# Optimization experiments

Measured on AMD Instinct MI355X. Metric: run time of the kernel, lower is better.

## Reference

```python
import jax, jax.numpy as jnp
import numpy as np

T, B, I, H = 1024, 64, 512, 512


def setup_inputs() -> dict:
    key = jax.random.key(0)
    ks = jax.random.split(key, 7)
    s = 1.0 / np.sqrt(H).astype(np.float32)
    return {
        "x": jax.random.normal(ks[0], (T, B, I), dtype=jnp.float32),
        "h0": jax.random.normal(ks[1], (B, H), dtype=jnp.float32),
        "c0": jax.random.normal(ks[2], (B, H), dtype=jnp.float32),
        "W_ih": jax.random.normal(ks[3], (4 * H, I), dtype=jnp.float32) * s,
        "W_hh": jax.random.normal(ks[4], (4 * H, H), dtype=jnp.float32) * s,
        "b_ih": jax.random.normal(ks[5], (4 * H,), dtype=jnp.float32) * s,
        "b_hh": jax.random.normal(ks[6], (4 * H,), dtype=jnp.float32) * s,
        "alpha": jnp.ones((1,), dtype=jnp.float32),
    }


def reference(x, h0, c0, W_ih, W_hh, b_ih, b_hh, alpha):
    # Precompute input-to-hidden projections for all timesteps in one GEMM.
    # x: [T, B, I] -> xg: [T, B, 4H]
    xg = jnp.einsum("tbi,gi->tbg", x, W_ih) + b_ih
    a = alpha[0]

    def step(carry, xg_t):
        h, c = carry  # [B, H] each
        gates = xg_t + h @ W_hh.T + b_hh  # [B, 4H]
        i, f, g, o = jnp.split(gates, 4, axis=-1)
        i = jax.nn.sigmoid(i)
        f = jax.nn.sigmoid(f)
        g = jnp.tanh(g)
        o = jax.nn.sigmoid(o)
        c_new = f * c + i * g
        h_new = o * jnp.tanh(c_new)
        # alpha step-size interpolation (alpha=1 -> plain LSTM)
        c_out = a * c_new + (1.0 - a) * c
        h_out = a * h_new + (1.0 - a) * h
        return (h_out, c_out), h_out

    (hT, cT), ys = jax.lax.scan(step, (h0, c0), xg)
    return ys, hT, cT
```

## Files before the change

### kernel.cpp

```cpp
#include <hip/hip_runtime.h>

typedef __attribute__((ext_vector_type(8))) short short8;
typedef __attribute__((ext_vector_type(4))) float f32x4;
typedef __attribute__((ext_vector_type(4))) float float4v;
typedef __attribute__((ext_vector_type(4))) unsigned short u16x4;
typedef __attribute__((ext_vector_type(4))) unsigned int u32x4;

#define T_TOT   1024
#define BATCH   64
#define HID     512
#define G4      2048
#define NGRID   128
#define BH      (BATCH * HID)

static __device__ __forceinline__ unsigned short f2bf(float x) {
  union { float f; unsigned u; } v; v.f = x;
  unsigned r = v.u + 0x7FFFu + ((v.u >> 16) & 1u);
  return (unsigned short)(r >> 16);
}
static __device__ __forceinline__ float sigm(float x) {
  return 1.0f / (1.0f + __expf(-x));
}
static __device__ __forceinline__ float tanh_fast(float x) {
  return 1.0f - 2.0f / (__expf(2.0f * x) + 1.0f);
}
static __device__ __forceinline__ void bar_lds() {
  asm volatile("s_waitcnt lgkmcnt(0)" ::: "memory");
  __builtin_amdgcn_s_barrier();
  asm volatile("" ::: "memory");
}

__global__ void init_k(const float* __restrict__ h0, const float* __restrict__ c0,
                       unsigned int* __restrict__ hb2, float* __restrict__ cst,
                       float* __restrict__ hst) {
  const int i = blockIdx.x * 256 + threadIdx.x;
  if (i < BH) {
    const float h = h0[i];
    hb2[i] = (unsigned)f2bf(h);
    hb2[BH + i] = 0xFFFF0000u;
    hst[i] = h;
    cst[i] = c0[i];
  }
}

static __device__ __forceinline__ void gemm_body(
    int bm, int bn, const float* __restrict__ A, const float* __restrict__ W,
    const float* __restrict__ bih, const float* __restrict__ bhh,
    float* __restrict__ xzp) {
  __shared__ unsigned short As[128 * 64];
  __shared__ unsigned short Bs[128 * 64];
  const int tid  = threadIdx.x;
  const int lane = tid & 63;
  const int wid  = tid >> 6;
  const int wm   = (wid >> 1) * 64;
  const int wn   = (wid & 1) * 64;
  const int l15  = lane & 15;
  const int l4   = lane >> 4;

  f32x4 acc[4][4];
#pragma unroll
  for (int mt = 0; mt < 4; ++mt)
#pragma unroll
    for (int nt = 0; nt < 4; ++nt) acc[mt][nt] = f32x4{0.f, 0.f, 0.f, 0.f};

  const float* Ab = A + (long)bm * 128 * 512;
  const float* Wb = W + (long)bn * 128 * 512;
  const int r0 = tid >> 4;
  const int cq = (tid & 15) * 4;

  for (int k0 = 0; k0 < 512; k0 += 64) {
#pragma unroll
    for (int pass = 0; pass < 8; ++pass) {
      const int r = pass * 16 + r0;
      const float4v va = *(const float4v*)(Ab + (long)r * 512 + k0 + cq);
      const float4v vb = *(const float4v*)(Wb + (long)r * 512 + k0 + cq);
      u16x4 pa, pb;
#pragma unroll
      for (int j = 0; j < 4; ++j) { pa[j] = f2bf(va[j]); pb[j] = f2bf(vb[j]); }
      const int boff = r * 128 + ((cq * 2) ^ ((r & 7) << 4));
      *(u16x4*)((char*)As + boff) = pa;
      *(u16x4*)((char*)Bs + boff) = pb;
    }
    __syncthreads();
#pragma unroll
    for (int kk = 0; kk < 2; ++kk) {
      short8 af[4], bfv[4];
#pragma unroll
      for (int mt = 0; mt < 4; ++mt) {
        const int row = wm + mt * 16 + l15;
        af[mt] = *(const short8*)((const char*)As + row * 128 +
                                  ((kk * 64 + l4 * 16) ^ ((row & 7) << 4)));
      }
#pragma unroll
      for (int nt = 0; nt < 4; ++nt) {
        const int row = wn + nt * 16 + l15;
        bfv[nt] = *(const short8*)((const char*)Bs + row * 128 +
                                   ((kk * 64 + l4 * 16) ^ ((row & 7) << 4)));
      }
#pragma unroll
      for (int mt = 0; mt < 4; ++mt)
#pragma unroll
        for (int nt = 0; nt < 4; ++nt)
          acc[mt][nt] = __builtin_amdgcn_mfma_f32_16x16x32_bf16(af[mt], bfv[nt], acc[mt][nt], 0, 0, 0);
    }
    __syncthreads();
  }

#pragma unroll
  for (int nt = 0; nt < 4; ++nt) {
    const int gn = bn * 128 + wn + nt * 16 + l15;
    const float bias = bih[gn] + bhh[gn];
    const int g2  = gn >> 9;
    const int hh  = gn & 511;
    const int nb2 = hh >> 4;
    const int en2 = hh & 15;
#pragma unroll
    for (int mt = 0; mt < 4; ++mt) {
      const int m0 = bm * 128 + wm + mt * 16 + l4 * 4;
#pragma unroll
      for (int r = 0; r < 4; ++r) {
        const int m = m0 + r;
        const int tt2 = m >> 6, brow = m & 63;
        const int mb2 = brow >> 4, em2 = brow & 15;
        xzp[((((size_t)tt2 * 4 + mb2) * 32 + nb2) << 10) + em2 * 64 + g2 * 16 + en2] =
            acc[mt][nt][r] + bias;
      }
    }
  }
}

__global__ __launch_bounds__(256) void xz_gemm(
    const float* __restrict__ A, const float* __restrict__ W,
    const float* __restrict__ bih, const float* __restrict__ bhh,
    float* __restrict__ xzp) {
  gemm_body(blockIdx.x, blockIdx.y, A, W, bih, bhh, xzp);
}

__global__ __launch_bounds__(256, 1) void fused_chunk(
    const float* __restrict__ xnext,
    const float* __restrict__ Wih,
    const float* __restrict__ bih, const float* __restrict__ bhh,
    float* __restrict__ xzp_next,
    const float* __restrict__ xzp_cur,
    const float* __restrict__ Whh,
    const float* __restrict__ alpha_p,
    float* __restrict__ out,
    unsigned int* __restrict__ hb2,
    float* __restrict__ cst, float* __restrict__ hst,
    int t0, int Tc) {
  const int bx = blockIdx.x;
  if (bx >= NGRID) {
    const int g = bx - NGRID;
    gemm_body(g >> 4, g & 15, xnext, Wih, bih, bhh, xzp_next);
    return;
  }

  const int mb  = bx >> 5;
  const int nb  = bx & 31;
  const int rb0 = mb * 16;
  const int hs0 = nb * 16;
  const int tid = threadIdx.x;
  const int lane = tid & 63;
  const int w   = tid >> 6;
  const int l15 = lane & 15;
  const int l4  = lane >> 4;

  __shared__ __align__(16) unsigned short h_lds[16 * HID];
  __shared__ __align__(16) float gates[4][16][20];

  short8 wf[16];
  {
    const float* wr = Whh + (long)(w * HID + hs0 + l15) * HID + l4 * 8;
#pragma unroll
    for (int ks = 0; ks < 16; ++ks) {
      const float4v lo = *(const float4v*)(wr + ks * 32);
      const float4v hi = *(const float4v*)(wr + ks * 32 + 4);
      short8 f;
#pragma unroll
      for (int j = 0; j < 4; ++j) {
        f[j]     = (short)f2bf(lo[j]);
        f[j + 4] = (short)f2bf(hi[j]);
      }
      wf[ks] = f;
    }
  }
  const float a = alpha_p[0];
  const float oma = 1.0f - a;

  const int em = tid >> 4;
  const int en = tid & 15;
  float cp = cst[(long)(rb0 + em) * HID + hs0 + en];
  float hp = hst[(long)(rb0 + em) * HID + hs0 + en];

  const long YS = (long)T_TOT * BATCH * HID;

  float xz0, xz1, xz2, xz3;
  u32x4 sa[4], sb[4];
  {
    const float* xb = xzp_cur + (((size_t)0 * 4 + mb) * 32 + nb) * 1024 + w * 16 + l15;
    asm volatile("global_load_dword %0, %1, off" : "=v"(xz0) : "v"(xb + (l4 * 4 + 0) * 64));
    asm volatile("global_load_dword %0, %1, off" : "=v"(xz1) : "v"(xb + (l4 * 4 + 1) * 64));
    asm volatile("global_load_dword %0, %1, off" : "=v"(xz2) : "v"(xb + (l4 * 4 + 2) * 64));
    asm volatile("global_load_dword %0, %1, off" : "=v"(xz3) : "v"(xb + (l4 * 4 + 3) * 64));
    const unsigned int* p0 = hb2 + (size_t)(t0 & 1) * BH + (size_t)(rb0 + w) * HID + lane * 8;
#pragma unroll
    for (int i = 0; i < 4; ++i) {
      const unsigned int* p = p0 + (size_t)i * 4 * HID;
      asm volatile("global_load_dwordx4 %0, %1, off sc0 sc1" : "=v"(sa[i]) : "v"(p));
      asm volatile("global_load_dwordx4 %0, %1, off sc0 sc1" : "=v"(sb[i]) : "v"(p + 4));
    }
  }

  for (int tt = 0; tt < Tc; ++tt) {
    const int t = t0 + tt;

    if (tt == 0) asm volatile("s_waitcnt vmcnt(0)" ::: "memory");
    else         asm volatile("s_waitcnt vmcnt(1)" ::: "memory");
    __builtin_amdgcn_sched_barrier(0);

    {
      const unsigned wantHi = ((unsigned)t) << 16;
      const unsigned int* p0 = hb2 + (size_t)(t & 1) * BH +
                               (size_t)(rb0 + w) * HID + lane * 8;
      for (;;) {
        unsigned bad = 0u;
#pragma unroll
        for (int i = 0; i < 4; ++i) {
          unsigned d = 0u;
#pragma unroll
          for (int j = 0; j < 4; ++j)
            d |= ((sa[i][j] ^ wantHi) | (sb[i][j] ^ wantHi));
          if (d & 0xFFFF0000u) bad |= (1u << i);
        }
        if (!__any(bad != 0u)) break;
#pragma unroll
        for (int i = 0; i < 4; ++i)
          if (bad & (1u << i)) {
            const unsigned int* p = p0 + (size_t)i * 4 * HID;
            asm volatile("global_load_dwordx4 %0, %1, off sc0 sc1" : "=v"(sa[i]) : "v"(p));
            asm volatile("global_load_dwordx4 %0, %1, off sc0 sc1" : "=v"(sb[i]) : "v"(p + 4));
          }
        asm volatile("s_waitcnt vmcnt(0)" ::: "memory");
        __builtin_amdgcn_sched_barrier(0);
      }
    }

#pragma unroll
    for (int i = 0; i < 4; ++i) {
      u32x4 pk;
      pk[0] = __builtin_amdgcn_perm(sa[i][1], sa[i][0], 0x05040100u);
      pk[1] = __builtin_amdgcn_perm(sa[i][3], sa[i][2], 0x05040100u);
      pk[2] = __builtin_amdgcn_perm(sb[i][1], sb[i][0], 0x05040100u);
      pk[3] = __builtin_amdgcn_perm(sb[i][3], sb[i][2], 0x05040100u);
      const int r = 4 * i + w;
      const int c = lane;
      *(u32x4*)((char*)h_lds + c * 256 + ((r ^ (c & 15)) << 4)) = pk;
    }
    bar_lds();

    f32x4 acc[4];
    acc[0][0] = xz0; acc[0][1] = xz1; acc[0][2] = xz2; acc[0][3] = xz3;
    acc[1] = f32x4{0.f, 0.f, 0.f, 0.f};
    acc[2] = acc[1];
    acc[3] = acc[1];
#pragma unroll
    for (int ks = 0; ks < 16; ++ks) {
      const int c = ks * 4 + l4;
      const short8 af = *(const short8*)((const char*)h_lds + c * 256 +
                                         ((l15 ^ (c & 15)) << 4));
      acc[ks & 3] = __builtin_amdgcn_mfma_f32_16x16x32_bf16(af, wf[ks], acc[ks & 3], 0, 0, 0);
    }
    {
      const f32x4 s = (acc[0] + acc[1]) + (acc[2] + acc[3]);
#pragma unroll
      for (int r = 0; r < 4; ++r)
        gates[w][l4 * 4 + r][l15] = s[r];
    }
    bar_lds();

    const float gi = gates[0][em][en], gf = gates[1][em][en];
    const float gg = gates[2][em][en], go = gates[3][em][en];
    const float ii = sigm(gi), ff = sigm(gf), oo = sigm(go);
    const float g  = tanh_fast(gg);
    const float cn = ff * cp + ii * g;
    const float hn = oo * tanh_fast(cn);
    const float co = a * cn + oma * cp;
    const float ho = a * hn + oma * hp;
    cp = co;
    hp = ho;

    {
      unsigned int* dst = hb2 + (size_t)((t + 1) & 1) * BH +
                          (long)(rb0 + em) * HID + hs0 + en;
      const unsigned w32 = (((unsigned)(t + 1)) << 16) | (unsigned)f2bf(ho);
      asm volatile("global_store_dword %0, %1, off sc0 sc1"
                   :: "v"((const void*)dst), "v"(w32) : "memory");
    }

    if (tt < Tc - 1) {
      const float* xb = xzp_cur + (((size_t)(tt + 1) * 4 + mb) * 32 + nb) * 1024 +
                        w * 16 + l15;
      asm volatile("global_load_dword %0, %1, off" : "=v"(xz0) : "v"(xb + (l4 * 4 + 0) * 64));
      asm volatile("global_load_dword %0, %1, off" : "=v"(xz1) : "v"(xb + (l4 * 4 + 1) * 64));
      asm volatile("global_load_dword %0, %1, off" : "=v"(xz2) : "v"(xb + (l4 * 4 + 2) * 64));
      asm volatile("global_load_dword %0, %1, off" : "=v"(xz3) : "v"(xb + (l4 * 4 + 3) * 64));
      const unsigned int* pn = hb2 + (size_t)((t + 1) & 1) * BH +
                               (size_t)(rb0 + w) * HID + lane * 8;
#pragma unroll
      for (int i = 0; i < 4; ++i) {
        const unsigned int* p = pn + (size_t)i * 4 * HID;
        asm volatile("global_load_dwordx4 %0, %1, off sc0 sc1" : "=v"(sa[i]) : "v"(p));
        asm volatile("global_load_dwordx4 %0, %1, off sc0 sc1" : "=v"(sb[i]) : "v"(p + 4));
      }
      const float* op = out + ((long)t * BATCH + rb0 + em) * HID + hs0 + en;
      asm volatile("global_store_dword %0, %1, off"
                   :: "v"((const void*)op), "v"(ho) : "memory");
    }
  }

  {
    const int tl = t0 + Tc - 1;
    out[((long)tl * BATCH + rb0 + em) * HID + hs0 + en] = hp;
    if (t0 + Tc == T_TOT) {
      out[YS + (long)(rb0 + em) * HID + hs0 + en] = hp;
      out[YS + BATCH * HID + (long)(rb0 + em) * HID + hs0 + en] = cp;
    }
    cst[(long)(rb0 + em) * HID + hs0 + en] = cp;
    hst[(long)(rb0 + em) * HID + hs0 + en] = hp;
  }
}

extern "C" void kernel_launch(void* const* d_in, const int* in_sizes, int n_in,
                              void* d_out, int out_size, void* d_ws, size_t ws_size,
                              hipStream_t stream) {
  const float* x     = (const float*)d_in[0];
  const float* h0    = (const float*)d_in[1];
  const float* c0    = (const float*)d_in[2];
  const float* W_ih  = (const float*)d_in[3];
  const float* W_hh  = (const float*)d_in[4];
  const float* b_ih  = (const float*)d_in[5];
  const float* b_hh  = (const float*)d_in[6];
  const float* alpha = (const float*)d_in[7];
  float* out = (float*)d_out;

  int Tc = 128;
  while ((size_t)2 * (size_t)Tc * 524288ull + 786432ull > ws_size && Tc > 2) Tc >>= 1;

  char* ws = (char*)d_ws;
  unsigned int* hb2 = (unsigned int*)(ws + 0);
  float* cst = (float*)(ws + 262144);
  float* hst = (float*)(ws + 393216);
  float* xzp0 = (float*)(ws + 786432);
  float* xzp1 = (float*)(ws + 786432 + (size_t)Tc * 524288ull);
  float* xzp[2] = {xzp0, xzp1};

  const int nchunk = T_TOT / Tc;
  const size_t xoff = (size_t)Tc * BATCH * 512;
  const int nG = (Tc / 2) * 16;

  init_k<<<128, 256, 0, stream>>>(h0, c0, hb2, cst, hst);
  {
    dim3 gg(Tc / 2, 16);
    xz_gemm<<<gg, 256, 0, stream>>>(x, W_ih, b_ih, b_hh, xzp[0]);
  }
  for (int k = 0; k < nchunk; ++k) {
    const bool last = (k == nchunk - 1);
    const int grid = NGRID + (last ? 0 : nG);
    fused_chunk<<<grid, 256, 0, stream>>>(
        x + (size_t)(k + 1) * xoff, W_ih, b_ih, b_hh, xzp[(k + 1) & 1],
        xzp[k & 1], W_hh, alpha, out, hb2, cst, hst, k * Tc, Tc);
  }
}
```

Before: 2.547 ms.

## Retile recurrent blocks to 8 batch rows by 32 hidden columns

Each persistent recurrent block now handles 8 batch rows and 32 hidden units instead of 16 by 16. That halves the per-step polled h traffic per block and doubles the register-resident W_hh fragments per wave. The xz projection layout is changed to match, and MFMA rows 8-15 are zero-padded in LDS, wasting half the matrix compute. The first h poll drops the sc1 cache bit, and a second plain store of the h word is added, possibly to speed up visibility of the flag.

```diff
diff --git a/kernel.cpp b/kernel.cpp
--- a/kernel.cpp
+++ b/kernel.cpp
@@ -110,10 +110,10 @@
   for (int nt = 0; nt < 4; ++nt) {
     const int gn = bn * 128 + wn + nt * 16 + l15;
     const float bias = bih[gn] + bhh[gn];
-    const int g2  = gn >> 9;
-    const int hh  = gn & 511;
-    const int nb2 = hh >> 4;
-    const int en2 = hh & 15;
+    const int g2   = gn >> 9;
+    const int hh   = gn & 511;
+    const int nb2  = hh >> 5;
+    const int col2 = hh & 31;
 #pragma unroll
     for (int mt = 0; mt < 4; ++mt) {
       const int m0 = bm * 128 + wm + mt * 16 + l4 * 4;
@@ -121,8 +121,8 @@
       for (int r = 0; r < 4; ++r) {
         const int m = m0 + r;
         const int tt2 = m >> 6, brow = m & 63;
-        const int mb2 = brow >> 4, em2 = brow & 15;
-        xzp[((((size_t)tt2 * 4 + mb2) * 32 + nb2) << 10) + em2 * 64 + g2 * 16 + en2] =
+        const int mb2 = brow >> 3, r2 = brow & 7;
+        xzp[((((size_t)tt2 * 8 + mb2) * 16 + nb2) << 10) + r2 * 128 + g2 * 32 + col2] =
             acc[mt][nt][r] + bias;
       }
     }
@@ -155,10 +155,10 @@
     return;
   }
 
-  const int mb  = bx >> 5;
-  const int nb  = bx & 31;
-  const int rb0 = mb * 16;
-  const int hs0 = nb * 16;
+  const int mb  = bx & 7;
+  const int nb  = bx >> 3;
+  const int rb0 = mb * 8;
+  const int hs0 = nb * 32;
   const int tid = threadIdx.x;
   const int lane = tid & 63;
   const int w   = tid >> 6;
@@ -166,49 +166,61 @@
   const int l4  = lane >> 4;
 
   __shared__ __align__(16) unsigned short h_lds[16 * HID];
-  __shared__ __align__(16) float gates[4][16][20];
-
-  short8 wf[16];
+  __shared__ __align__(16) float gates[4][16][36];
+
+  short8 wf0[16], wf1[16];
   {
-    const float* wr = Whh + (long)(w * HID + hs0 + l15) * HID + l4 * 8;
+    const float* wr0 = Whh + (long)(w * HID + hs0 + l15) * HID + l4 * 8;
+    const float* wr1 = Whh + (long)(w * HID + hs0 + 16 + l15) * HID + l4 * 8;
 #pragma unroll
     for (int ks = 0; ks < 16; ++ks) {
-      const float4v lo = *(const float4v*)(wr + ks * 32);
-      const float4v hi = *(const float4v*)(wr + ks * 32 + 4);
+      float4v lo = *(const float4v*)(wr0 + ks * 32);
+      float4v hi = *(const float4v*)(wr0 + ks * 32 + 4);
       short8 f;
 #pragma unroll
-      for (int j = 0; j < 4; ++j) {
-        f[j]     = (short)f2bf(lo[j]);
-        f[j + 4] = (short)f2bf(hi[j]);
-      }
-      wf[ks] = f;
+      for (int j = 0; j < 4; ++j) { f[j] = (short)f2bf(lo[j]); f[j+4] = (short)f2bf(hi[j]); }
+      wf0[ks] = f;
+      lo = *(const float4v*)(wr1 + ks * 32);
+      hi = *(const float4v*)(wr1 + ks * 32 + 4);
+#pragma unroll
+      for (int j = 0; j < 4; ++j) { f[j] = (short)f2bf(lo[j]); f[j+4] = (short)f2bf(hi[j]); }
+      wf1[ks] = f;
     }
   }
   const float a = alpha_p[0];
   const float oma = 1.0f - a;
 
-  const int em = tid >> 4;
-  const int en = tid & 15;
+  for (int idx = tid; idx < 512; idx += 256) {
+    const int r = 8 + (idx >> 6), c = idx & 63;
+    *(u32x4*)((char*)h_lds + c * 256 + ((r ^ (c & 15)) << 4)) = u32x4{0u,0u,0u,0u};
+  }
+
+  const int em = tid >> 5;
+  const int en = tid & 31;
   float cp = cst[(long)(rb0 + em) * HID + hs0 + en];
   float hp = hst[(long)(rb0 + em) * HID + hs0 + en];
+  bar_lds();
 
   const long YS = (long)T_TOT * BATCH * HID;
-
-  float xz0, xz1, xz2, xz3;
-  u32x4 sa[4], sb[4];
+  const int swr = tid >> 5;
+  const int swc = (tid & 31) * 16;
+
+  float xzv[8];
+  u32x4 sv[4];
   {
-    const float* xb = xzp_cur + (((size_t)0 * 4 + mb) * 32 + nb) * 1024 + w * 16 + l15;
-    asm volatile("global_load_dword %0, %1, off" : "=v"(xz0) : "v"(xb + (l4 * 4 + 0) * 64));
-    asm volatile("global_load_dword %0, %1, off" : "=v"(xz1) : "v"(xb + (l4 * 4 + 1) * 64));
-    asm volatile("global_load_dword %0, %1, off" : "=v"(xz2) : "v"(xb + (l4 * 4 + 2) * 64));
-    asm volatile("global_load_dword %0, %1, off" : "=v"(xz3) : "v"(xb + (l4 * 4 + 3) * 64));
-    const unsigned int* p0 = hb2 + (size_t)(t0 & 1) * BH + (size_t)(rb0 + w) * HID + lane * 8;
-#pragma unroll
-    for (int i = 0; i < 4; ++i) {
-      const unsigned int* p = p0 + (size_t)i * 4 * HID;
-      asm volatile("global_load_dwordx4 %0, %1, off sc0 sc1" : "=v"(sa[i]) : "v"(p));
-      asm volatile("global_load_dwordx4 %0, %1, off sc0 sc1" : "=v"(sb[i]) : "v"(p + 4));
-    }
+    const float* xb = xzp_cur + ((((size_t)0 * 8 + mb) * 16 + nb) << 10);
+#pragma unroll
+    for (int n = 0; n < 2; ++n)
+#pragma unroll
+      for (int j = 0; j < 4; ++j) {
+        const float* p = xb + ((l4 * 4 + j) & 7) * 128 + w * 32 + n * 16 + l15;
+        asm volatile("global_load_dword %0, %1, off" : "=v"(xzv[n*4+j]) : "v"(p));
+      }
+    const unsigned int* p0 = hb2 + (size_t)(t0 & 1) * BH +
+                             (size_t)(rb0 + swr) * HID + swc;
+#pragma unroll
+    for (int i = 0; i < 4; ++i)
+      asm volatile("global_load_dwordx4 %0, %1, off sc0" : "=v"(sv[i]) : "v"(p0 + i * 4));
   }
 
   for (int tt = 0; tt < Tc; ++tt) {
@@ -221,60 +233,65 @@
     {
       const unsigned wantHi = ((unsigned)t) << 16;
       const unsigned int* p0 = hb2 + (size_t)(t & 1) * BH +
-                               (size_t)(rb0 + w) * HID + lane * 8;
+                               (size_t)(rb0 + swr) * HID + swc;
       for (;;) {
         unsigned bad = 0u;
 #pragma unroll
         for (int i = 0; i < 4; ++i) {
           unsigned d = 0u;
 #pragma unroll
-          for (int j = 0; j < 4; ++j)
-            d |= ((sa[i][j] ^ wantHi) | (sb[i][j] ^ wantHi));
+          for (int j = 0; j < 4; ++j) d |= (sv[i][j] ^ wantHi);
           if (d & 0xFFFF0000u) bad |= (1u << i);
         }
         if (!__any(bad != 0u)) break;
 #pragma unroll
         for (int i = 0; i < 4; ++i)
-          if (bad & (1u << i)) {
-            const unsigned int* p = p0 + (size_t)i * 4 * HID;
-            asm volatile("global_load_dwordx4 %0, %1, off sc0 sc1" : "=v"(sa[i]) : "v"(p));
-            asm volatile("global_load_dwordx4 %0, %1, off sc0 sc1" : "=v"(sb[i]) : "v"(p + 4));
-          }
+          if (bad & (1u << i))
+            asm volatile("global_load_dwordx4 %0, %1, off sc0 sc1"
+                         : "=v"(sv[i]) : "v"(p0 + i * 4));
         asm volatile("s_waitcnt vmcnt(0)" ::: "memory");
         __builtin_amdgcn_sched_barrier(0);
       }
     }
 
 #pragma unroll
-    for (int i = 0; i < 4; ++i) {
+    for (int q = 0; q < 2; ++q) {
       u32x4 pk;
-      pk[0] = __builtin_amdgcn_perm(sa[i][1], sa[i][0], 0x05040100u);
-      pk[1] = __builtin_amdgcn_perm(sa[i][3], sa[i][2], 0x05040100u);
-      pk[2] = __builtin_amdgcn_perm(sb[i][1], sb[i][0], 0x05040100u);
-      pk[3] = __builtin_amdgcn_perm(sb[i][3], sb[i][2], 0x05040100u);
-      const int r = 4 * i + w;
-      const int c = lane;
-      *(u32x4*)((char*)h_lds + c * 256 + ((r ^ (c & 15)) << 4)) = pk;
+      pk[0] = __builtin_amdgcn_perm(sv[q*2][1],   sv[q*2][0],   0x05040100u);
+      pk[1] = __builtin_amdgcn_perm(sv[q*2][3],   sv[q*2][2],   0x05040100u);
+      pk[2] = __builtin_amdgcn_perm(sv[q*2+1][1], sv[q*2+1][0], 0x05040100u);
+      pk[3] = __builtin_amdgcn_perm(sv[q*2+1][3], sv[q*2+1][2], 0x05040100u);
+      const int c = (tid & 31) * 2 + q;
+      *(u32x4*)((char*)h_lds + c * 256 + ((swr ^ (c & 15)) << 4)) = pk;
     }
     bar_lds();
 
-    f32x4 acc[4];
-    acc[0][0] = xz0; acc[0][1] = xz1; acc[0][2] = xz2; acc[0][3] = xz3;
-    acc[1] = f32x4{0.f, 0.f, 0.f, 0.f};
-    acc[2] = acc[1];
-    acc[3] = acc[1];
-#pragma unroll
-    for (int ks = 0; ks < 16; ++ks) {
-      const int c = ks * 4 + l4;
-      const short8 af = *(const short8*)((const char*)h_lds + c * 256 +
-                                         ((l15 ^ (c & 15)) << 4));
-      acc[ks & 3] = __builtin_amdgcn_mfma_f32_16x16x32_bf16(af, wf[ks], acc[ks & 3], 0, 0, 0);
+    f32x4 ac00, ac01, ac10, ac11;
+    ac00 = f32x4{xzv[0], xzv[1], xzv[2], xzv[3]};
+    ac10 = f32x4{xzv[4], xzv[5], xzv[6], xzv[7]};
+    ac01 = f32x4{0.f, 0.f, 0.f, 0.f};
+    ac11 = ac01;
+#pragma unroll
+    for (int ks = 0; ks < 16; ks += 2) {
+      const int c0 = ks * 4 + l4;
+      const int c1 = c0 + 4;
+      const short8 af0 = *(const short8*)((const char*)h_lds + c0 * 256 +
+                                          ((l15 ^ (c0 & 15)) << 4));
+      const short8 af1 = *(const short8*)((const char*)h_lds + c1 * 256 +
+                                          ((l15 ^ (c1 & 15)) << 4));
+      ac00 = __builtin_amdgcn_mfma_f32_16x16x32_bf16(af0, wf0[ks],   ac00, 0, 0, 0);
+      ac10 = __builtin_amdgcn_mfma_f32_16x16x32_bf16(af0, wf1[ks],   ac10, 0, 0, 0);
+      ac01 = __builtin_amdgcn_mfma_f32_16x16x32_bf16(af1, wf0[ks+1], ac01, 0, 0, 0);
+      ac11 = __builtin_amdgcn_mfma_f32_16x16x32_bf16(af1, wf1[ks+1], ac11, 0, 0, 0);
     }
     {
-      const f32x4 s = (acc[0] + acc[1]) + (acc[2] + acc[3]);
-#pragma unroll
-      for (int r = 0; r < 4; ++r)
-        gates[w][l4 * 4 + r][l15] = s[r];
+      const f32x4 s0 = ac00 + ac01;
+      const f32x4 s1 = ac10 + ac11;
+#pragma unroll
+      for (int r = 0; r < 4; ++r) {
+        gates[w][l4 * 4 + r][l15]      = s0[r];
+        gates[w][l4 * 4 + r][16 + l15] = s1[r];
+      }
     }
     bar_lds();
 
@@ -295,23 +312,24 @@
       const unsigned w32 = (((unsigned)(t + 1)) << 16) | (unsigned)f2bf(ho);
       asm volatile("global_store_dword %0, %1, off sc0 sc1"
                    :: "v"((const void*)dst), "v"(w32) : "memory");
+      asm volatile("global_store_dword %0, %1, off"
+                   :: "v"((const void*)dst), "v"(w32) : "memory");
     }
 
     if (tt < Tc - 1) {
-      const float* xb = xzp_cur + (((size_t)(tt + 1) * 4 + mb) * 32 + nb) * 1024 +
-                        w * 16 + l15;
-      asm volatile("global_load_dword %0, %1, off" : "=v"(xz0) : "v"(xb + (l4 * 4 + 0) * 64));
-      asm volatile("global_load_dword %0, %1, off" : "=v"(xz1) : "v"(xb + (l4 * 4 + 1) * 64));
-      asm volatile("global_load_dword %0, %1, off" : "=v"(xz2) : "v"(xb + (l4 * 4 + 2) * 64));
-      asm volatile("global_load_dword %0, %1, off" : "=v"(xz3) : "v"(xb + (l4 * 4 + 3) * 64));
+      const float* xb = xzp_cur + ((((size_t)(tt + 1) * 8 + mb) * 16 + nb) << 10);
+#pragma unroll
+      for (int n = 0; n < 2; ++n)
+#pragma unroll
+        for (int j = 0; j < 4; ++j) {
+          const float* p = xb + ((l4 * 4 + j) & 7) * 128 + w * 32 + n * 16 + l15;
+          asm volatile("global_load_dword %0, %1, off" : "=v"(xzv[n*4+j]) : "v"(p));
+        }
       const unsigned int* pn = hb2 + (size_t)((t + 1) & 1) * BH +
-                               (size_t)(rb0 + w) * HID + lane * 8;
-#pragma unroll
-      for (int i = 0; i < 4; ++i) {
-        const unsigned int* p = pn + (size_t)i * 4 * HID;
-        asm volatile("global_load_dwordx4 %0, %1, off sc0 sc1" : "=v"(sa[i]) : "v"(p));
-        asm volatile("global_load_dwordx4 %0, %1, off sc0 sc1" : "=v"(sb[i]) : "v"(p + 4));
-      }
+                               (size_t)(rb0 + swr) * HID + swc;
+#pragma unroll
+      for (int i = 0; i < 4; ++i)
+        asm volatile("global_load_dwordx4 %0, %1, off sc0" : "=v"(sv[i]) : "v"(pn + i * 4));
       const float* op = out + ((long)t * BATCH + rb0 + em) * HID + hs0 + en;
       asm volatile("global_store_dword %0, %1, off"
                    :: "v"((const void*)op), "v"(ho) : "memory");
```

Result: faster. 2.444 ms (median of 2 runs) (-4.1%).
